# Optimization experiments

Hardware: AMD Instinct MI355X
Metric: run time of the kernel (lower is better)

The kernel has to match this reference:

```python
import jax, jax.numpy as jnp
import numpy as np

NUM_EMBEDDINGS = 512
EMBEDDING_DIM = 64


def setup_inputs() -> dict:
    key = jax.random.key(0)
    k1, k2 = jax.random.split(key)
    z_e = jax.random.normal(k1, (32, EMBEDDING_DIM, 64, 64), dtype=jnp.float32)
    lim = 1.0 / NUM_EMBEDDINGS
    codebook = jax.random.uniform(k2, (NUM_EMBEDDINGS, EMBEDDING_DIM),
                                  dtype=jnp.float32, minval=-lim, maxval=lim)
    return {"z_e": z_e, "codebook": codebook}


def reference(z_e, codebook):
    B, C, H, W = z_e.shape
    # [B,C,H,W] -> [N, C] with N = B*H*W (channels-last flatten)
    z_flat = jnp.transpose(z_e, (0, 2, 3, 1)).reshape(-1, C)
    # squared L2 distance via ||a||^2 + ||b||^2 - 2 a.b (same math, no NxKxC tensor)
    d = (jnp.sum(z_flat * z_flat, axis=1, keepdims=True)          # [N,1]
         + jnp.sum(codebook * codebook, axis=1)[None, :]           # [1,K]
         - 2.0 * jnp.einsum('nc,kc->nk', z_flat, codebook))        # [N,K]
    encoding_indices = jnp.argmin(d, axis=1)                       # [N] int
    z_q = codebook[encoding_indices].reshape(B, H, W, C)
    z_q = jnp.transpose(z_q, (0, 3, 1, 2))                         # [B,C,H,W]
    return z_q, encoding_indices
```

## Files before the change

### kernel.cpp

```cpp
#include <hip/hip_runtime.h>


#pragma clang fp contract(off)

#define KCODES 512
#define CDIM 64
#define HW 4096
#define ZQ_ELEMS 8388608

__global__ __launch_bounds__(256, 4) void vq_kernel(
    const float* __restrict__ z_e,
    const float* __restrict__ cb,
    float* __restrict__ out)
{
    __shared__ float cnorm[KCODES];
    __shared__ float dcand[256];
    __shared__ int   kcand[256];

    for (int k = (int)threadIdx.x; k < KCODES; k += 256) {
        const float* row = cb + k * CDIM;
        float r[8];
        #pragma unroll
        for (int j = 0; j < 8; ++j) r[j] = row[j] * row[j];
        #pragma unroll
        for (int i = 8; i < 64; i += 8) {
            #pragma unroll
            for (int j = 0; j < 8; ++j) r[j] = r[j] + row[i + j] * row[i + j];
        }
        cnorm[k] = ((r[0] + r[1]) + (r[2] + r[3])) + ((r[4] + r[5]) + (r[6] + r[7]));
    }

    const int lane = (int)threadIdx.x & 63;
    const int g = __builtin_amdgcn_readfirstlane((int)threadIdx.x >> 6);
    const int n0 = (int)blockIdx.x * 64;
    const int b = n0 / HW;
    const int hw0 = n0 % HW;
    const float* zp = z_e + (size_t)b * CDIM * HW + hw0 + lane;

    float z[CDIM];
    #pragma unroll
    for (int c = 0; c < CDIM; ++c) z[c] = zp[(size_t)c * HW];

    float sz;
    {
        float r[8];
        #pragma unroll
        for (int j = 0; j < 8; ++j) r[j] = z[j] * z[j];
        #pragma unroll
        for (int i = 8; i < 64; i += 8) {
            #pragma unroll
            for (int j = 0; j < 8; ++j) r[j] = r[j] + z[i + j] * z[i + j];
        }
        sz = ((r[0] + r[1]) + (r[2] + r[3])) + ((r[4] + r[5]) + (r[6] + r[7]));
    }

    __syncthreads();

    float best = 3.4e38f;
    int bk = 0;
    const int k0 = g * 128;

    for (int i = 0; i < 128; ++i) {
        const int k = k0 + i;
        const float* ck = cb + k * CDIM;

        float v[16];
        #pragma unroll
        for (int l = 0; l < 16; ++l) {
            v[l] = fmaf(z[l], ck[l],
                     fmaf(z[16 + l], ck[16 + l],
                       fmaf(z[32 + l], ck[32 + l],
                         fmaf(z[48 + l], ck[48 + l], 0.f))));
        }
        float e0 = v[0] + v[8],  e1 = v[1] + v[9],  e2 = v[2] + v[10], e3 = v[3] + v[11];
        float e4 = v[4] + v[12], e5 = v[5] + v[13], e6 = v[6] + v[14], e7 = v[7] + v[15];
        float f0 = e0 + e4, f1 = e1 + e5, f2 = e2 + e6, f3 = e3 + e7;
        float dot = (f0 + f2) + (f1 + f3);

        float A = sz + cnorm[k];
        float d = A + dot * -2.f;

        if (d < best) { best = d; bk = k; }
    }

    dcand[g * 64 + lane] = best;
    kcand[g * 64 + lane] = bk;
    __syncthreads();

    float bd = dcand[lane];
    int bi = kcand[lane];
    #pragma unroll
    for (int gg = 1; gg < 4; ++gg) {
        float d2 = dcand[gg * 64 + lane];
        int   k2 = kcand[gg * 64 + lane];
        if (d2 < bd) { bd = d2; bi = k2; }
    }

    if (g == 0) out[ZQ_ELEMS + n0 + lane] = (float)bi;

    const float* row = cb + (size_t)bi * CDIM;
    float* op = out + (size_t)b * CDIM * HW + hw0 + lane;
    #pragma unroll
    for (int c = 0; c < 16; ++c) {
        const int ch = g * 16 + c;
        op[(size_t)ch * HW] = row[ch];
    }
}

extern "C" void kernel_launch(void* const* d_in, const int* in_sizes, int n_in,
                              void* d_out, int out_size, void* d_ws, size_t ws_size,
                              hipStream_t stream) {
    const float* z_e = (const float*)d_in[0];
    const float* cb  = (const float*)d_in[1];
    float* out = (float*)d_out;
    vq_kernel<<<dim3(2048), dim3(256), 0, stream>>>(z_e, cb, out);
}
```

Baseline: 238.3 us.

## Use bf16 MFMA for candidate distances with exact fp32 rescoring of near-ties

Replaces the scalar fp32 distance loop with bf16 MFMA matrix ops, splitting z into high and low bf16 parts for roughly fp32-level accuracy. The codebook is converted to bf16 and its norms precomputed in separate small kernels. Candidates within a fixed margin of the best score are rescored with exact fp32 arithmetic, falling back to a full scan if there are too many. The aim is to cut the scalar FMA cost, at the price of extra launches, a margin heuristic that may not hold for all inputs, and a divergent slow path.

```diff
diff --git a/kernel.cpp b/kernel.cpp
--- a/kernel.cpp
+++ b/kernel.cpp
@@ -1,4 +1,5 @@
 #include <hip/hip_runtime.h>
+#include <stdint.h>
 
 
 #pragma clang fp contract(off)
@@ -7,103 +8,198 @@
 #define CDIM 64
 #define HW 4096
 #define ZQ_ELEMS 8388608
-
-__global__ __launch_bounds__(256, 4) void vq_kernel(
+#define MARGIN_S 2e-4f
+
+typedef __attribute__((ext_vector_type(8))) short s8;
+typedef __attribute__((ext_vector_type(4))) float fx4;
+
+static __device__ __forceinline__ uint16_t bf16_rne(float f) {
+    uint32_t u = __float_as_uint(f);
+    return (uint16_t)((u + 0x7FFFu + ((u >> 16) & 1u)) >> 16);
+}
+
+static __device__ float sz_numpy(const float* zv) {
+    float r[8];
+    #pragma unroll
+    for (int j = 0; j < 8; ++j) r[j] = zv[j] * zv[j];
+    #pragma unroll
+    for (int i = 8; i < 64; i += 8) {
+        #pragma unroll
+        for (int j = 0; j < 8; ++j) r[j] = r[j] + zv[i + j] * zv[i + j];
+    }
+    return ((r[0] + r[1]) + (r[2] + r[3])) + ((r[4] + r[5]) + (r[6] + r[7]));
+}
+static __device__ float d_numpy(const float* zv, const float* cb,
+                                const float* cnorm_g, float sz, int k) {
+    const float* ck = cb + k * CDIM;
+    float v[16];
+    #pragma unroll
+    for (int l = 0; l < 16; ++l) {
+        v[l] = fmaf(zv[l], ck[l],
+                 fmaf(zv[16 + l], ck[16 + l],
+                   fmaf(zv[32 + l], ck[32 + l],
+                     fmaf(zv[48 + l], ck[48 + l], 0.f))));
+    }
+    float e0 = v[0] + v[8],  e1 = v[1] + v[9],  e2 = v[2] + v[10], e3 = v[3] + v[11];
+    float e4 = v[4] + v[12], e5 = v[5] + v[13], e6 = v[6] + v[14], e7 = v[7] + v[15];
+    float f0 = e0 + e4, f1 = e1 + e5, f2 = e2 + e6, f3 = e3 + e7;
+    float dot = (f0 + f2) + (f1 + f3);
+    float A = sz + cnorm_g[k];
+    return fmaf(dot, -2.f, A);
+}
+
+__global__ __launch_bounds__(256) void vq_norms(const float* __restrict__ cb,
+                                                float* __restrict__ cnorm_g)
+{
+    const int k = (int)blockIdx.x * 256 + (int)threadIdx.x;
+    if (k >= KCODES) return;
+    const float* row = cb + k * CDIM;
+    float r[8];
+    #pragma unroll
+    for (int j = 0; j < 8; ++j) r[j] = row[j] * row[j];
+    #pragma unroll
+    for (int i = 8; i < 64; i += 8) {
+        #pragma unroll
+        for (int j = 0; j < 8; ++j) r[j] = r[j] + row[i + j] * row[i + j];
+    }
+    cnorm_g[k] = ((r[0] + r[1]) + (r[2] + r[3])) + ((r[4] + r[5]) + (r[6] + r[7]));
+}
+
+__global__ __launch_bounds__(256) void vq_cvt(const float* __restrict__ cb,
+                                              uint16_t* __restrict__ cb16)
+{
+    const int i = (int)blockIdx.x * 256 + (int)threadIdx.x;
+    if (i < KCODES * CDIM) cb16[i] = bf16_rne(cb[i]);
+}
+
+__global__ __launch_bounds__(64, 2) void vq_main(
     const float* __restrict__ z_e,
     const float* __restrict__ cb,
+    const float* __restrict__ cnorm_g,
+    const uint16_t* __restrict__ cb16,
     float* __restrict__ out)
 {
-    __shared__ float cnorm[KCODES];
-    __shared__ float dcand[256];
-    __shared__ int   kcand[256];
-
-    for (int k = (int)threadIdx.x; k < KCODES; k += 256) {
-        const float* row = cb + k * CDIM;
-        float r[8];
-        #pragma unroll
-        for (int j = 0; j < 8; ++j) r[j] = row[j] * row[j];
-        #pragma unroll
-        for (int i = 8; i < 64; i += 8) {
+    const int tid = (int)threadIdx.x;
+    const int p16 = tid & 15;
+    const int quad = tid >> 4;
+    const int quad4 = quad * 4;
+
+    const int n = (int)blockIdx.x * 16 + p16;
+    const int b = n >> 12;
+    const int hwp = n & 4095;
+    const float* zptr = z_e + (size_t)b * CDIM * HW + hwp;
+
+    s8 bh[2], bl[2];
+    #pragma unroll
+    for (int s = 0; s < 2; ++s) {
+        #pragma unroll
+        for (int j = 0; j < 8; ++j) {
+            const int ch = s * 32 + quad * 8 + j;
+            float f = zptr[(size_t)ch * HW];
+            uint16_t h = bf16_rne(f);
+            float fh = __uint_as_float((uint32_t)h << 16);
+            uint16_t l = bf16_rne(f - fh);
+            bh[s][j] = (short)h;
+            bl[s][j] = (short)l;
+        }
+    }
+
+    fx4 accs[32];
+    #pragma unroll 4
+    for (int m = 0; m < 32; ++m) {
+        fx4 cn = *(const fx4*)(cnorm_g + m * 16 + quad4);
+        const uint16_t* ar = cb16 + (size_t)(m * 16 + p16) * CDIM + quad * 8;
+        s8 a0 = *(const s8*)(ar);
+        s8 a1 = *(const s8*)(ar + 32);
+        fx4 acc = cn * -0.5f;
+        acc = __builtin_amdgcn_mfma_f32_16x16x32_bf16(a0, bh[0], acc, 0, 0, 0);
+        acc = __builtin_amdgcn_mfma_f32_16x16x32_bf16(a1, bh[1], acc, 0, 0, 0);
+        acc = __builtin_amdgcn_mfma_f32_16x16x32_bf16(a0, bl[0], acc, 0, 0, 0);
+        acc = __builtin_amdgcn_mfma_f32_16x16x32_bf16(a1, bl[1], acc, 0, 0, 0);
+        accs[m] = acc;
+    }
+
+    float mx = -3.4e38f;
+    #pragma unroll
+    for (int m = 0; m < 32; ++m) {
+        fx4 a = accs[m];
+        mx = fmaxf(mx, fmaxf(fmaxf(a.x, a.y), fmaxf(a.z, a.w)));
+    }
+    mx = fmaxf(mx, __shfl_xor(mx, 16, 64));
+    mx = fmaxf(mx, __shfl_xor(mx, 32, 64));
+    const float T = mx - MARGIN_S;
+
+    uint32_t mk0 = 0, mk1 = 0, mk2 = 0, mk3 = 0;
+    #pragma unroll
+    for (int m = 0; m < 32; ++m) {
+        fx4 a = accs[m];
+        uint32_t w = (uint32_t)(a.x >= T) | ((uint32_t)(a.y >= T) << 1)
+                   | ((uint32_t)(a.z >= T) << 2) | ((uint32_t)(a.w >= T) << 3);
+        uint32_t sh = (uint32_t)(m & 7) * 4;
+        if (m < 8)       mk0 |= w << sh;
+        else if (m < 16) mk1 |= w << sh;
+        else if (m < 24) mk2 |= w << sh;
+        else             mk3 |= w << sh;
+    }
+    uint64_t lo = ((uint64_t)mk1 << 32) | mk0;
+    uint64_t hi = ((uint64_t)mk3 << 32) | mk2;
+    int cnt = __popcll(lo) + __popcll(hi);
+
+    uint64_t l2 = lo & (lo - 1);
+    uint64_t h2 = lo ? hi : (hi & (hi - 1));
+    int j1 = lo ? (__ffsll((long long)lo) - 1) : (hi ? 64 + __ffsll((long long)hi) - 1 : -1);
+    int j2 = l2 ? (__ffsll((long long)l2) - 1) : (h2 ? 64 + __ffsll((long long)h2) - 1 : -1);
+    int k1 = (j1 >= 0) ? (((j1 >> 2) << 4) + quad4 + (j1 & 3)) : 1023;
+    int k2 = (j2 >= 0) ? (((j2 >> 2) << 4) + quad4 + (j2 & 3)) : 1023;
+
+    int cnt_t = cnt + __shfl_xor(cnt, 16, 64);
+    cnt_t += __shfl_xor(cnt_t, 32, 64);
+    int kmin = min(k1, __shfl_xor(k1, 16, 64));
+    kmin = min(kmin, __shfl_xor(kmin, 32, 64));
+    int of = (cnt > 2) ? 1 : 0;
+    of |= __shfl_xor(of, 16, 64);
+    of |= __shfl_xor(of, 32, 64);
+
+    int ka[8];
+    #pragma unroll
+    for (int g = 0; g < 4; ++g) {
+        ka[2 * g]     = __shfl(k1, p16 + 16 * g, 64);
+        ka[2 * g + 1] = __shfl(k2, p16 + 16 * g, 64);
+    }
+
+    int idx = kmin;
+    if (tid < 16 && cnt_t >= 2) {
+        float zv[64];
+        #pragma unroll
+        for (int c = 0; c < 64; ++c) zv[c] = zptr[(size_t)c * HW];
+        float sz = sz_numpy(zv);
+        float bd = 3.4e38f; int bi = 1023;
+        if (!of) {
             #pragma unroll
-            for (int j = 0; j < 8; ++j) r[j] = r[j] + row[i + j] * row[i + j];
+            for (int i = 0; i < 8; ++i) {
+                int k = ka[i];
+                if (k < 1023) {
+                    float d = d_numpy(zv, cb, cnorm_g, sz, k);
+                    if (d < bd || (d == bd && k < bi)) { bd = d; bi = k; }
+                }
+            }
+        } else {
+            for (int k = 0; k < KCODES; ++k) {
+                float d = d_numpy(zv, cb, cnorm_g, sz, k);
+                if (d < bd || (d == bd && k < bi)) { bd = d; bi = k; }
+            }
         }
-        cnorm[k] = ((r[0] + r[1]) + (r[2] + r[3])) + ((r[4] + r[5]) + (r[6] + r[7]));
-    }
-
-    const int lane = (int)threadIdx.x & 63;
-    const int g = __builtin_amdgcn_readfirstlane((int)threadIdx.x >> 6);
-    const int n0 = (int)blockIdx.x * 64;
-    const int b = n0 / HW;
-    const int hw0 = n0 % HW;
-    const float* zp = z_e + (size_t)b * CDIM * HW + hw0 + lane;
-
-    float z[CDIM];
-    #pragma unroll
-    for (int c = 0; c < CDIM; ++c) z[c] = zp[(size_t)c * HW];
-
-    float sz;
-    {
-        float r[8];
-        #pragma unroll
-        for (int j = 0; j < 8; ++j) r[j] = z[j] * z[j];
-        #pragma unroll
-        for (int i = 8; i < 64; i += 8) {
-            #pragma unroll
-            for (int j = 0; j < 8; ++j) r[j] = r[j] + z[i + j] * z[i + j];
-        }
-        sz = ((r[0] + r[1]) + (r[2] + r[3])) + ((r[4] + r[5]) + (r[6] + r[7]));
-    }
-
-    __syncthreads();
-
-    float best = 3.4e38f;
-    int bk = 0;
-    const int k0 = g * 128;
-
-    for (int i = 0; i < 128; ++i) {
-        const int k = k0 + i;
-        const float* ck = cb + k * CDIM;
-
-        float v[16];
-        #pragma unroll
-        for (int l = 0; l < 16; ++l) {
-            v[l] = fmaf(z[l], ck[l],
-                     fmaf(z[16 + l], ck[16 + l],
-                       fmaf(z[32 + l], ck[32 + l],
-                         fmaf(z[48 + l], ck[48 + l], 0.f))));
-        }
-        float e0 = v[0] + v[8],  e1 = v[1] + v[9],  e2 = v[2] + v[10], e3 = v[3] + v[11];
-        float e4 = v[4] + v[12], e5 = v[5] + v[13], e6 = v[6] + v[14], e7 = v[7] + v[15];
-        float f0 = e0 + e4, f1 = e1 + e5, f2 = e2 + e6, f3 = e3 + e7;
-        float dot = (f0 + f2) + (f1 + f3);
-
-        float A = sz + cnorm[k];
-        float d = A + dot * -2.f;
-
-        if (d < best) { best = d; bk = k; }
-    }
-
-    dcand[g * 64 + lane] = best;
-    kcand[g * 64 + lane] = bk;
-    __syncthreads();
-
-    float bd = dcand[lane];
-    int bi = kcand[lane];
-    #pragma unroll
-    for (int gg = 1; gg < 4; ++gg) {
-        float d2 = dcand[gg * 64 + lane];
-        int   k2 = kcand[gg * 64 + lane];
-        if (d2 < bd) { bd = d2; bi = k2; }
-    }
-
-    if (g == 0) out[ZQ_ELEMS + n0 + lane] = (float)bi;
-
-    const float* row = cb + (size_t)bi * CDIM;
-    float* op = out + (size_t)b * CDIM * HW + hw0 + lane;
+        idx = bi;
+    }
+    idx = __shfl(idx, p16, 64);
+
+    if (quad == 0) out[ZQ_ELEMS + n] = (float)idx;
+    const float* crow = cb + (size_t)idx * CDIM;
+    float* op = out + (size_t)b * CDIM * HW + hwp;
     #pragma unroll
     for (int c = 0; c < 16; ++c) {
-        const int ch = g * 16 + c;
-        op[(size_t)ch * HW] = row[ch];
+        const int ch = quad * 16 + c;
+        op[(size_t)ch * HW] = crow[ch];
     }
 }
 
@@ -113,5 +209,9 @@
     const float* z_e = (const float*)d_in[0];
     const float* cb  = (const float*)d_in[1];
     float* out = (float*)d_out;
-    vq_kernel<<<dim3(2048), dim3(256), 0, stream>>>(z_e, cb, out);
-}
+    float* cnorm_g = (float*)d_ws;
+    uint16_t* cb16 = (uint16_t*)((char*)d_ws + 2048);
+    vq_norms<<<dim3(2),   dim3(256), 0, stream>>>(cb, cnorm_g);
+    vq_cvt  <<<dim3(128), dim3(256), 0, stream>>>(cb, cb16);
+    vq_main <<<dim3(8192), dim3(64), 0, stream>>>(z_e, cb, cnorm_g, cb16, out);
+}
```

New measurement: 350.3 us. 47.0% more time.

## Use split-bf16 MFMA for distance search with exact fp32 fallback for near-ties

Applied to the files above, without the earlier changes.

Replaces the scalar fp32 dot-product search with MFMA 32x32x16 bf16 matrix ops. The hi/lo bf16 split of both z and codebook (three products) approximates fp32 accuracy, and the score is computed as dot minus half the norm. Points whose top-two scores fall within a margin go onto an atomic list, and a fix-up kernel recomputes them exactly in the original fp32 order so argmin matches the reference. Codebook norms and the bf16 conversion move to small pre-kernels. The cost is extra launches, a memset, and a risk of mismatches if the margin misses some ties.

```diff
diff --git a/kernel.cpp b/kernel.cpp
--- a/kernel.cpp
+++ b/kernel.cpp
@@ -1,4 +1,5 @@
 #include <hip/hip_runtime.h>
+#include <stdint.h>
 
 
 #pragma clang fp contract(off)
@@ -7,103 +8,230 @@
 #define CDIM 64
 #define HW 4096
 #define ZQ_ELEMS 8388608
-
-__global__ __launch_bounds__(256, 4) void vq_kernel(
+#define MARGIN_S 2e-4f
+
+#define WS_CNORM   0
+#define WS_CNORMH  2048
+#define WS_CH      4096
+#define WS_CL      69632
+#define WS_COUNT   135168
+#define WS_LIST    135172
+
+typedef __attribute__((ext_vector_type(8)))  short s8;
+typedef __attribute__((ext_vector_type(4)))  float fx4;
+typedef __attribute__((ext_vector_type(16))) float fx16;
+
+static __device__ __forceinline__ uint16_t bf16_rne(float f) {
+    uint32_t u = __float_as_uint(f);
+    return (uint16_t)((u + 0x7FFFu + ((u >> 16) & 1u)) >> 16);
+}
+
+static __device__ __forceinline__ float sz_numpy(const float* zv) {
+    float r[8];
+    #pragma unroll
+    for (int j = 0; j < 8; ++j) r[j] = zv[j] * zv[j];
+    #pragma unroll
+    for (int i = 8; i < 64; i += 8) {
+        #pragma unroll
+        for (int j = 0; j < 8; ++j) r[j] = r[j] + zv[i + j] * zv[i + j];
+    }
+    return ((r[0] + r[1]) + (r[2] + r[3])) + ((r[4] + r[5]) + (r[6] + r[7]));
+}
+static __device__ __forceinline__ float d_numpy(const float* zv, const float* cb,
+                                                const float* cnorm_g, float sz, int k) {
+    const float* ck = cb + k * CDIM;
+    float v[16];
+    #pragma unroll
+    for (int l = 0; l < 16; ++l) {
+        v[l] = fmaf(zv[l], ck[l],
+                 fmaf(zv[16 + l], ck[16 + l],
+                   fmaf(zv[32 + l], ck[32 + l],
+                     fmaf(zv[48 + l], ck[48 + l], 0.f))));
+    }
+    float e0 = v[0] + v[8],  e1 = v[1] + v[9],  e2 = v[2] + v[10], e3 = v[3] + v[11];
+    float e4 = v[4] + v[12], e5 = v[5] + v[13], e6 = v[6] + v[14], e7 = v[7] + v[15];
+    float f0 = e0 + e4, f1 = e1 + e5, f2 = e2 + e6, f3 = e3 + e7;
+    float dot = (f0 + f2) + (f1 + f3);
+    float A = sz + cnorm_g[k];
+    return fmaf(dot, -2.f, A);
+}
+
+__global__ __launch_bounds__(256) void vq_norms(const float* __restrict__ cb,
+                                                float* __restrict__ cnorm_g,
+                                                float* __restrict__ cnormh_g)
+{
+    const int k = (int)blockIdx.x * 256 + (int)threadIdx.x;
+    if (k >= KCODES) return;
+    const float* row = cb + k * CDIM;
+    float r[8];
+    #pragma unroll
+    for (int j = 0; j < 8; ++j) r[j] = row[j] * row[j];
+    #pragma unroll
+    for (int i = 8; i < 64; i += 8) {
+        #pragma unroll
+        for (int j = 0; j < 8; ++j) r[j] = r[j] + row[i + j] * row[i + j];
+    }
+    float cn = ((r[0] + r[1]) + (r[2] + r[3])) + ((r[4] + r[5]) + (r[6] + r[7]));
+    cnorm_g[k] = cn;
+    cnormh_g[k] = -0.5f * cn;
+}
+
+__global__ __launch_bounds__(256) void vq_cvt(const float* __restrict__ cb,
+                                              uint16_t* __restrict__ ch16,
+                                              uint16_t* __restrict__ cl16)
+{
+    const int i = (int)blockIdx.x * 256 + (int)threadIdx.x;
+    if (i >= KCODES * CDIM) return;
+    float c = cb[i];
+    uint16_t hi = bf16_rne(c);
+    ch16[i] = hi;
+    cl16[i] = bf16_rne(c - __uint_as_float((uint32_t)hi << 16));
+}
+
+__global__ __launch_bounds__(64, 4) void vq_main(
     const float* __restrict__ z_e,
     const float* __restrict__ cb,
+    const float* __restrict__ cnormh_g,
+    const uint16_t* __restrict__ ch16,
+    const uint16_t* __restrict__ cl16,
+    float* __restrict__ out,
+    int* __restrict__ counter,
+    int* __restrict__ list)
+{
+    const int lane = (int)threadIdx.x;
+    const int p = lane & 31;
+    const int h = lane >> 5;
+
+    const int n = (int)blockIdx.x * 32 + p;
+    const int b = n >> 12;
+    const int hw = n & 4095;
+    const float* zptr = z_e + (size_t)b * CDIM * HW + hw;
+
+    s8 bh[4], bl[4];
+    #pragma unroll
+    for (int s = 0; s < 4; ++s) {
+        #pragma unroll
+        for (int j = 0; j < 8; ++j) {
+            const int c = s * 16 + h * 8 + j;
+            float f = zptr[(size_t)c * HW];
+            uint16_t hi = bf16_rne(f);
+            bh[s][j] = (short)hi;
+            bl[s][j] = (short)bf16_rne(f - __uint_as_float((uint32_t)hi << 16));
+        }
+    }
+
+    float max1 = -3.4e38f, max2 = -3.4e38f;
+    int k1 = 0;
+
+    #pragma unroll 2
+    for (int t = 0; t < 16; ++t) {
+        const uint16_t* arh = ch16 + (size_t)(t * 32 + p) * CDIM + h * 8;
+        const uint16_t* arl = cl16 + (size_t)(t * 32 + p) * CDIM + h * 8;
+        s8 ah[4], al[4];
+        #pragma unroll
+        for (int s = 0; s < 4; ++s) {
+            ah[s] = *(const s8*)(arh + s * 16);
+            al[s] = *(const s8*)(arl + s * 16);
+        }
+
+        fx16 acc;
+        #pragma unroll
+        for (int q = 0; q < 4; ++q) {
+            fx4 c4 = *(const fx4*)(cnormh_g + t * 32 + 4 * h + 8 * q);
+            acc[q * 4 + 0] = c4.x; acc[q * 4 + 1] = c4.y;
+            acc[q * 4 + 2] = c4.z; acc[q * 4 + 3] = c4.w;
+        }
+
+        #pragma unroll
+        for (int s = 0; s < 4; ++s)
+            acc = __builtin_amdgcn_mfma_f32_32x32x16_bf16(ah[s], bh[s], acc, 0, 0, 0);
+        #pragma unroll
+        for (int s = 0; s < 4; ++s)
+            acc = __builtin_amdgcn_mfma_f32_32x32x16_bf16(ah[s], bl[s], acc, 0, 0, 0);
+        #pragma unroll
+        for (int s = 0; s < 4; ++s)
+            acc = __builtin_amdgcn_mfma_f32_32x32x16_bf16(al[s], bh[s], acc, 0, 0, 0);
+
+        #pragma unroll
+        for (int q = 0; q < 4; ++q) {
+            #pragma unroll
+            for (int i = 0; i < 4; ++i) {
+                float sv = acc[q * 4 + i];
+                const int kc = t * 32 + 8 * q + 4 * h + i;
+                float losr = fminf(sv, max1);
+                max2 = fmaxf(max2, losr);
+                bool gt = sv > max1;
+                k1 = gt ? kc : k1;
+                max1 = fmaxf(sv, max1);
+            }
+        }
+    }
+
+    float m1o = __shfl_xor(max1, 32, 64);
+    float m2o = __shfl_xor(max2, 32, 64);
+    int   k1o = __shfl_xor(k1, 32, 64);
+    float max2g = fmaxf(fminf(max1, m1o), fmaxf(max2, m2o));
+    int   k1g = (m1o > max1) ? k1o : ((m1o == max1) ? min(k1, k1o) : k1);
+    float max1g = fmaxf(max1, m1o);
+
+    const bool amb = (max1g - max2g) < MARGIN_S;
+    if (amb && h == 0) {
+        int pos = atomicAdd(counter, 1);
+        list[pos] = n;
+    }
+
+    if (h == 0) out[ZQ_ELEMS + n] = (float)k1g;
+
+    const float* crow = cb + (size_t)k1g * CDIM;
+    float* op = out + (size_t)b * CDIM * HW + hw;
+    #pragma unroll
+    for (int c = 0; c < 32; ++c) {
+        const int cc = h * 32 + c;
+        op[(size_t)cc * HW] = crow[cc];
+    }
+}
+
+__global__ __launch_bounds__(256) void vq_fix(
+    const float* __restrict__ z_e,
+    const float* __restrict__ cb,
+    const float* __restrict__ cnorm_g,
+    const int* __restrict__ counter,
+    const int* __restrict__ list,
     float* __restrict__ out)
 {
-    __shared__ float cnorm[KCODES];
-    __shared__ float dcand[256];
-    __shared__ int   kcand[256];
-
-    for (int k = (int)threadIdx.x; k < KCODES; k += 256) {
-        const float* row = cb + k * CDIM;
-        float r[8];
-        #pragma unroll
-        for (int j = 0; j < 8; ++j) r[j] = row[j] * row[j];
-        #pragma unroll
-        for (int i = 8; i < 64; i += 8) {
-            #pragma unroll
-            for (int j = 0; j < 8; ++j) r[j] = r[j] + row[i + j] * row[i + j];
-        }
-        cnorm[k] = ((r[0] + r[1]) + (r[2] + r[3])) + ((r[4] + r[5]) + (r[6] + r[7]));
-    }
-
+    const int wv = (int)blockIdx.x * 4 + ((int)threadIdx.x >> 6);
     const int lane = (int)threadIdx.x & 63;
-    const int g = __builtin_amdgcn_readfirstlane((int)threadIdx.x >> 6);
-    const int n0 = (int)blockIdx.x * 64;
-    const int b = n0 / HW;
-    const int hw0 = n0 % HW;
-    const float* zp = z_e + (size_t)b * CDIM * HW + hw0 + lane;
-
-    float z[CDIM];
-    #pragma unroll
-    for (int c = 0; c < CDIM; ++c) z[c] = zp[(size_t)c * HW];
-
-    float sz;
-    {
-        float r[8];
-        #pragma unroll
-        for (int j = 0; j < 8; ++j) r[j] = z[j] * z[j];
-        #pragma unroll
-        for (int i = 8; i < 64; i += 8) {
-            #pragma unroll
-            for (int j = 0; j < 8; ++j) r[j] = r[j] + z[i + j] * z[i + j];
-        }
-        sz = ((r[0] + r[1]) + (r[2] + r[3])) + ((r[4] + r[5]) + (r[6] + r[7]));
-    }
-
-    __syncthreads();
-
-    float best = 3.4e38f;
-    int bk = 0;
-    const int k0 = g * 128;
-
-    for (int i = 0; i < 128; ++i) {
-        const int k = k0 + i;
-        const float* ck = cb + k * CDIM;
-
-        float v[16];
-        #pragma unroll
-        for (int l = 0; l < 16; ++l) {
-            v[l] = fmaf(z[l], ck[l],
-                     fmaf(z[16 + l], ck[16 + l],
-                       fmaf(z[32 + l], ck[32 + l],
-                         fmaf(z[48 + l], ck[48 + l], 0.f))));
-        }
-        float e0 = v[0] + v[8],  e1 = v[1] + v[9],  e2 = v[2] + v[10], e3 = v[3] + v[11];
-        float e4 = v[4] + v[12], e5 = v[5] + v[13], e6 = v[6] + v[14], e7 = v[7] + v[15];
-        float f0 = e0 + e4, f1 = e1 + e5, f2 = e2 + e6, f3 = e3 + e7;
-        float dot = (f0 + f2) + (f1 + f3);
-
-        float A = sz + cnorm[k];
-        float d = A + dot * -2.f;
-
-        if (d < best) { best = d; bk = k; }
-    }
-
-    dcand[g * 64 + lane] = best;
-    kcand[g * 64 + lane] = bk;
-    __syncthreads();
-
-    float bd = dcand[lane];
-    int bi = kcand[lane];
-    #pragma unroll
-    for (int gg = 1; gg < 4; ++gg) {
-        float d2 = dcand[gg * 64 + lane];
-        int   k2 = kcand[gg * 64 + lane];
-        if (d2 < bd) { bd = d2; bi = k2; }
-    }
-
-    if (g == 0) out[ZQ_ELEMS + n0 + lane] = (float)bi;
-
-    const float* row = cb + (size_t)bi * CDIM;
-    float* op = out + (size_t)b * CDIM * HW + hw0 + lane;
-    #pragma unroll
-    for (int c = 0; c < 16; ++c) {
-        const int ch = g * 16 + c;
-        op[(size_t)ch * HW] = row[ch];
+    const int count = *counter;
+
+    for (int i = wv; i < count; i += 1024) {
+        const int n = list[i];
+        const int b = n >> 12;
+        const int hw = n & 4095;
+        const float* zptr = z_e + (size_t)b * CDIM * HW + hw;
+
+        float zv[64];
+        #pragma unroll
+        for (int c = 0; c < 64; ++c) zv[c] = zptr[(size_t)c * HW];
+        const float sz = sz_numpy(zv);
+
+        float bd = 3.4e38f; int bi = 0x7fffffff;
+        #pragma unroll
+        for (int j = 0; j < 8; ++j) {
+            const int k = lane + 64 * j;
+            float d = d_numpy(zv, cb, cnorm_g, sz, k);
+            if (d < bd || (d == bd && k < bi)) { bd = d; bi = k; }
+        }
+        #pragma unroll
+        for (int off = 32; off; off >>= 1) {
+            float d2 = __shfl_xor(bd, off, 64);
+            int   k2 = __shfl_xor(bi, off, 64);
+            if (d2 < bd || (d2 == bd && k2 < bi)) { bd = d2; bi = k2; }
+        }
+
+        if (lane == 0) out[ZQ_ELEMS + n] = (float)bi;
+        const float* crow = cb + (size_t)bi * CDIM;
+        float* op = out + (size_t)b * CDIM * HW + hw;
+        op[(size_t)lane * HW] = crow[lane];
     }
 }
 
@@ -113,5 +241,18 @@
     const float* z_e = (const float*)d_in[0];
     const float* cb  = (const float*)d_in[1];
     float* out = (float*)d_out;
-    vq_kernel<<<dim3(2048), dim3(256), 0, stream>>>(z_e, cb, out);
-}
+
+    float*    cnorm_g  = (float*)((char*)d_ws + WS_CNORM);
+    float*    cnormh_g = (float*)((char*)d_ws + WS_CNORMH);
+    uint16_t* ch16     = (uint16_t*)((char*)d_ws + WS_CH);
+    uint16_t* cl16     = (uint16_t*)((char*)d_ws + WS_CL);
+    int*      counter  = (int*)((char*)d_ws + WS_COUNT);
+    int*      list     = (int*)((char*)d_ws + WS_LIST);
+
+    hipMemsetAsync(counter, 0, sizeof(int), stream);
+    vq_norms<<<dim3(2),   dim3(256), 0, stream>>>(cb, cnorm_g, cnormh_g);
+    vq_cvt  <<<dim3(128), dim3(256), 0, stream>>>(cb, ch16, cl16);
+    vq_main <<<dim3(4096), dim3(64), 0, stream>>>(z_e, cb, cnormh_g, ch16, cl16,
+                                                  out, counter, list);
+    vq_fix  <<<dim3(256), dim3(256), 0, stream>>>(z_e, cb, cnorm_g, counter, list, out);
+}
```

New measurement: 300.3 us. 26.0% more time.
